# Optimization experiments

Measured on AMD Instinct MI355X. Metric: run time of the kernel, lower is better.

## Reference

```python
import jax, jax.numpy as jnp
import numpy as np

N_NODES = 50000
N_EDGES = 600000
DIM = 128
VOCAB = 512
PAD_ID = 0
LN_EPS = 1e-5


def setup_inputs() -> dict:
    key = jax.random.key(0)
    ks = jax.random.split(key, 8)
    node_ids = jax.random.randint(ks[0], (N_NODES,), 0, VOCAB, dtype=jnp.int32)
    edge_index = jax.random.randint(ks[1], (2, N_EDGES), 0, N_NODES, dtype=jnp.int32)
    edge_weight = jax.random.uniform(ks[2], (N_EDGES,), dtype=jnp.float32)
    # embedding with padding row zeroed (padding_idx semantics)
    emb = jax.random.normal(ks[3], (VOCAB, DIM), dtype=jnp.float32) * 0.05
    emb = emb.at[PAD_ID].set(0.0)
    s = 1.0 / np.sqrt(DIM)
    W1 = jax.random.normal(ks[4], (DIM, DIM), dtype=jnp.float32) * s
    b1 = jnp.zeros((DIM,), jnp.float32)
    W2 = jax.random.normal(ks[5], (DIM, DIM), dtype=jnp.float32) * s
    b2 = jnp.zeros((DIM,), jnp.float32)
    return {
        "node_ids": node_ids, "edge_index": edge_index, "edge_weight": edge_weight,
        "emb": emb, "W1": W1, "b1": b1, "W2": W2, "b2": b2,
        "gamma1": jnp.ones((DIM,), jnp.float32), "beta1": jnp.zeros((DIM,), jnp.float32),
        "gamma2": jnp.ones((DIM,), jnp.float32), "beta2": jnp.zeros((DIM,), jnp.float32),
    }


def _gcn_conv(x, row, col, ew, W, b, n_nodes):
    """PyG GCNConv: normalize=True, add_self_loops=True, improved=False.
    Aggregation j->i: edge (row=src j, col=dst i)."""
    h = x @ W  # [N, out]
    # add self loops with weight 1
    loop = jnp.arange(n_nodes, dtype=row.dtype)
    row_f = jnp.concatenate([row, loop])
    col_f = jnp.concatenate([col, loop])
    ew_f = jnp.concatenate([ew, jnp.ones((n_nodes,), ew.dtype)])
    # symmetric degree normalization (deg over destination index)
    deg = jax.ops.segment_sum(ew_f, col_f, num_segments=n_nodes)
    dis = jnp.where(deg > 0, jax.lax.rsqrt(jnp.maximum(deg, 1e-12)), 0.0)
    norm = dis[row_f] * ew_f * dis[col_f]  # [E+N]
    msg = norm[:, None] * h[row_f]  # gather + scale  [E+N, out]
    out = jax.ops.segment_sum(msg, col_f, num_segments=n_nodes)  # scatter-add
    return out + b


def _layer_norm(x, gamma, beta):
    mu = jnp.mean(x, axis=-1, keepdims=True)
    var = jnp.mean(jnp.square(x - mu), axis=-1, keepdims=True)
    return (x - mu) * jax.lax.rsqrt(var + LN_EPS) * gamma + beta


def reference(node_ids, edge_index, edge_weight, emb, W1, b1, W2, b2,
              gamma1, beta1, gamma2, beta2):
    row, col = edge_index[0], edge_index[1]
    x = emb[node_ids]  # [N, D]
    x1 = _gcn_conv(x, row, col, edge_weight, W1, b1, N_NODES)
    x = _layer_norm(x + x1, gamma1, beta1)  # dropout is identity in eval
    x2 = _gcn_conv(x, row, col, edge_weight, W2, b2, N_NODES)
    x = _layer_norm(x + x2, gamma2, beta2)
    return x
```

## Files before the change

### kernel.cpp

```cpp
#include <hip/hip_runtime.h>

#define N_NODES 50000
#define N_EDGES 600000
#define DIM     128
#define VOCAB   512
#define LN_EPS  1e-5f
#define FIXS    16777216.0f

typedef unsigned int uint;
typedef unsigned long long ull;
typedef unsigned short ushort;
typedef __attribute__((ext_vector_type(8))) short s8v;
typedef __attribute__((ext_vector_type(4))) float f4v;
typedef __attribute__((ext_vector_type(4))) int   i4v;
typedef __attribute__((ext_vector_type(4))) uint  u4v;
typedef __attribute__((ext_vector_type(2))) int   i2v;
typedef __attribute__((ext_vector_type(4))) float fv4;
typedef __attribute__((ext_vector_type(2))) float f2v;

__device__ __forceinline__ uint f2bf(float f) {
    uint u = __float_as_uint(f);
    return (u + 0x7fffu + ((u >> 16) & 1u)) >> 16;
}
__device__ __forceinline__ float bf_lo(uint p) { return __uint_as_float(p << 16); }
__device__ __forceinline__ float bf_hi(uint p) { return __uint_as_float(p & 0xffff0000u); }

__global__ void deg_rank_kernel(const int* __restrict__ ei, const float* __restrict__ ew,
                                ull* pack, ushort* __restrict__ rank, int E) {
    int e0 = (blockIdx.x * blockDim.x + threadIdx.x) * 8;
    if (e0 >= E) return;
    i4v c0 = __builtin_nontemporal_load((const i4v*)(ei + E + e0));
    i4v c1 = __builtin_nontemporal_load((const i4v*)(ei + E + e0 + 4));
    fv4 w0 = __builtin_nontemporal_load((const fv4*)(ew + e0));
    fv4 w1 = __builtin_nontemporal_load((const fv4*)(ew + e0 + 4));
    int   c[8] = {c0.x, c0.y, c0.z, c0.w, c1.x, c1.y, c1.z, c1.w};
    float w[8] = {w0.x, w0.y, w0.z, w0.w, w1.x, w1.y, w1.z, w1.w};
    ull r[8];
    #pragma unroll
    for (int k = 0; k < 8; k++) {
        ull a = (1ull << 32) | (ull)(uint)__float2int_rn(w[k] * FIXS);
        r[k] = atomicAdd(&pack[c[k]], a);
    }
    u4v o;
    o.x = (uint)(r[0] >> 32) | ((uint)(r[1] >> 32) << 16);
    o.y = (uint)(r[2] >> 32) | ((uint)(r[3] >> 32) << 16);
    o.z = (uint)(r[4] >> 32) | ((uint)(r[5] >> 32) << 16);
    o.w = (uint)(r[6] >> 32) | ((uint)(r[7] >> 32) << 16);
    __builtin_nontemporal_store(o, (u4v*)(rank + e0));
}

__global__ void scan_a(const ull* __restrict__ pack,
                       float* dis, int* row_ptr, int* bsum, int n) {
    __shared__ int sd[1024];
    int t = threadIdx.x;
    int i = blockIdx.x * 1024 + t;
    int v = 0;
    if (i < n) {
        ull pv = pack[i];
        v = (int)(pv >> 32);
        dis[i] = rsqrtf(1.0f + (float)(uint)(pv & 0xffffffffu) * (1.0f / FIXS));
    }
    sd[t] = v;
    __syncthreads();
    for (int off = 1; off < 1024; off <<= 1) {
        int add = (t >= off) ? sd[t - off] : 0;
        __syncthreads();
        sd[t] += add;
        __syncthreads();
    }
    if (i < n) row_ptr[i] = sd[t] - v;
    if (t == 1023) bsum[blockIdx.x] = sd[t];
}

__global__ void scan_c(int* row_ptr, const int* __restrict__ bsum,
                       int n, int E, int nb) {
    __shared__ int ofs_s;
    int t = threadIdx.x;
    if (t < 64) {
        int v = (t < nb && t < (int)blockIdx.x) ? bsum[t] : 0;
        #pragma unroll
        for (int o = 32; o > 0; o >>= 1) v += __shfl_xor(v, o, 64);
        if (t == 0) ofs_s = v;
    }
    __syncthreads();
    int i = blockIdx.x * 1024 + t;
    if (i < n) row_ptr[i] += ofs_s;
    if (i == 0) row_ptr[n] = E;
}

__global__ void scatter_kernel(const int* __restrict__ ei, const float* __restrict__ ew,
                               const float* __restrict__ dis, const int* __restrict__ nid,
                               const int* __restrict__ row_ptr, const ushort* __restrict__ rank,
                               int2* __restrict__ epack, int E) {
    int e = blockIdx.x * blockDim.x + threadIdx.x;
    if (e < E) {
        int s = ei[e];
        int c = ei[E + e];
        int pos = row_ptr[c] + (int)rank[e];
        uint ids = (uint)s | ((uint)nid[s] << 16);
        float wp = dis[s] * ew[e];
        i2v rec = {(int)ids, __float_as_int(wp)};
        __builtin_nontemporal_store(rec, (i2v*)(epack + pos));
    }
}

__global__ __launch_bounds__(256) void mm1_prepack(const float* __restrict__ X,
                                                   const float* __restrict__ W,
                                                   uint* __restrict__ Hb, int M,
                                                   const float* __restrict__ W2,
                                                   ushort* __restrict__ Wp) {
    __shared__ float Wt[32 * 128];
    __shared__ float Xt[64 * 36];
    int tid = threadIdx.x;
    int nmm = (M + 63) / 64;
    if ((int)blockIdx.x >= nmm) {
        int o = (blockIdx.x - nmm) * 256 + tid;
        int j = o & 7, lane = (o >> 3) & 63, chunk = o >> 9;
        int kc = chunk & 3, nc = chunk >> 2;
        int k = kc * 32 + (lane >> 4) * 8 + j;
        int n = nc * 16 + (lane & 15);
        Wp[o] = (ushort)f2bf(W2[k * 128 + n]);
        return;
    }
    int tx = tid & 31, ty = tid >> 5;
    int r0 = blockIdx.x * 64;
    float acc[8][4];
    #pragma unroll
    for (int j = 0; j < 8; j++)
        #pragma unroll
        for (int c = 0; c < 4; c++) acc[j][c] = 0.f;

    for (int kb = 0; kb < 128; kb += 32) {
        __syncthreads();
        #pragma unroll
        for (int q = 0; q < 4; q++) {
            int f = q * 256 + tid;
            ((float4*)Wt)[f] = *(const float4*)(W + kb * 128 + f * 4);
        }
        #pragma unroll
        for (int q = 0; q < 2; q++) {
            int f = q * 256 + tid;
            int row = f >> 3, cs = f & 7;
            int gr = r0 + row;
            float4 xv = make_float4(0.f, 0.f, 0.f, 0.f);
            if (gr < M) xv = *(const float4*)(X + (size_t)gr * 128 + kb + cs * 4);
            *(float4*)(Xt + row * 36 + cs * 4) = xv;
        }
        __syncthreads();
        #pragma unroll
        for (int k = 0; k < 32; k += 4) {
            float wv[4][4];
            #pragma unroll
            for (int kk = 0; kk < 4; kk++) {
                float4 t4 = *(const float4*)(Wt + (k + kk) * 128 + tx * 4);
                wv[kk][0] = t4.x; wv[kk][1] = t4.y; wv[kk][2] = t4.z; wv[kk][3] = t4.w;
            }
            #pragma unroll
            for (int j = 0; j < 8; j++) {
                float4 xv = *(const float4*)(Xt + (ty * 8 + j) * 36 + k);
                float xs[4] = {xv.x, xv.y, xv.z, xv.w};
                #pragma unroll
                for (int kk = 0; kk < 4; kk++)
                    #pragma unroll
                    for (int c = 0; c < 4; c++)
                        acc[j][c] = fmaf(xs[kk], wv[kk][c], acc[j][c]);
            }
        }
    }
    #pragma unroll
    for (int j = 0; j < 8; j++) {
        int gr = r0 + ty * 8 + j;
        if (gr < M) {
            uint p0 = f2bf(acc[j][0]) | (f2bf(acc[j][1]) << 16);
            uint p1 = f2bf(acc[j][2]) | (f2bf(acc[j][3]) << 16);
            ((uint2*)Hb)[(size_t)gr * 32 + tx] = make_uint2(p0, p1);
        }
    }
}

__global__ __launch_bounds__(256) void mm2_mfma(const uint* __restrict__ Xb,
                                                const ushort* __restrict__ Wp,
                                                ushort* __restrict__ H, int M) {
    int wid = (blockIdx.x * 256 + threadIdx.x) >> 6;
    int lane = threadIdx.x & 63;
    int r0 = wid * 16;
    if (r0 >= M) return;
    int quad = lane >> 4, lo = lane & 15;
    const uint* xrow = Xb + (size_t)(r0 + lo) * 64 + quad * 4;
    s8v a[4];
    #pragma unroll
    for (int kc = 0; kc < 4; kc++) a[kc] = *(const s8v*)(xrow + kc * 16);
    #pragma unroll
    for (int nc = 0; nc < 8; nc++) {
        f4v acc = {0.f, 0.f, 0.f, 0.f};
        #pragma unroll
        for (int kc = 0; kc < 4; kc++) {
            s8v b = *(const s8v*)(Wp + (size_t)((nc * 4 + kc) * 64 + lane) * 8);
            acc = __builtin_amdgcn_mfma_f32_16x16x32_bf16(a[kc], b, acc, 0, 0, 0);
        }
        ushort* hp = H + (size_t)(r0 + quad * 4) * 128 + nc * 16 + lo;
        #pragma unroll
        for (int r = 0; r < 4; r++)
            hp[(size_t)r * 128] = (ushort)f2bf(acc[r]);
    }
}

template<int SHIFT, bool RESID_BF, bool OUT_BF>
__global__ __launch_bounds__(256) void agg_ln(const int* __restrict__ row_ptr,
                                              const int2* __restrict__ epack,
                                              const float* __restrict__ dis,
                                              const uint* __restrict__ hb,
                                              const int* __restrict__ nid,
                                              const void* __restrict__ resid,
                                              const float* __restrict__ bias,
                                              const float* __restrict__ gamma,
                                              const float* __restrict__ beta,
                                              void* __restrict__ out, int n) {
    int i = (blockIdx.x * 256 + threadIdx.x) >> 6;
    int lane = threadIdx.x & 63;
    if (i >= n) return;
    int iw = __builtin_amdgcn_readfirstlane(i);
    int hri = nid ? nid[iw] : iw;
    float dl = dis[iw];
    uint ps = hb[(size_t)hri * 64 + lane];
    float sx[4] = {dl * bf_lo(ps), 0.f, 0.f, 0.f};
    float sy[4] = {dl * bf_hi(ps), 0.f, 0.f, 0.f};
    int e0 = row_ptr[iw], e1 = row_ptr[iw + 1];
    for (int j = e0; j < e1; j += 8) {
        i2v er[8];
        #pragma unroll
        for (int k = 0; k < 8; k++) {
            int idx = (j + k < e1) ? j + k : e0;
            er[k] = __builtin_nontemporal_load((const i2v*)(epack + idx));
        }
        uint qv[8];
        #pragma unroll
        for (int k = 0; k < 8; k++)
            qv[k] = hb[(size_t)(((uint)er[k].x >> SHIFT) & 0xffffu) * 64 + lane];
        #pragma unroll
        for (int k = 0; k < 8; k++) {
            float w = (j + k < e1) ? __int_as_float(er[k].y) : 0.f;
            sx[k & 3] += w * bf_lo(qv[k]);
            sy[k & 3] += w * bf_hi(qv[k]);
        }
    }
    float acc0 = (sx[0] + sx[1]) + (sx[2] + sx[3]);
    float acc1 = (sy[0] + sy[1]) + (sy[2] + sy[3]);
    float2 xr;
    if (RESID_BF) {
        uint pr = __builtin_nontemporal_load((const uint*)resid + (size_t)hri * 64 + lane);
        xr = make_float2(bf_lo(pr), bf_hi(pr));
    } else {
        xr = ((const float2*)resid)[(size_t)hri * 64 + lane];
    }
    float2 bi = ((const float2*)bias)[lane];
    float v0 = xr.x + dl * acc0 + bi.x;
    float v1 = xr.y + dl * acc1 + bi.y;
    float s1 = v0 + v1, s2 = v0 * v0 + v1 * v1;
    #pragma unroll
    for (int o = 32; o > 0; o >>= 1) {
        s1 += __shfl_xor(s1, o, 64);
        s2 += __shfl_xor(s2, o, 64);
    }
    float mu   = s1 * (1.0f / DIM);
    float var  = s2 * (1.0f / DIM) - mu * mu;
    float rstd = rsqrtf(var + LN_EPS);
    float2 ga = ((const float2*)gamma)[lane];
    float2 be = ((const float2*)beta)[lane];
    float o0 = (v0 - mu) * rstd * ga.x + be.x;
    float o1 = (v1 - mu) * rstd * ga.y + be.y;
    if (OUT_BF) {
        __builtin_nontemporal_store(f2bf(o0) | (f2bf(o1) << 16),
                                    (uint*)out + (size_t)i * 64 + lane);
    } else {
        f2v ov = {o0, o1};
        __builtin_nontemporal_store(ov, (f2v*)((float2*)out + (size_t)i * 64 + lane));
    }
}

extern "C" void kernel_launch(void* const* d_in, const int* in_sizes, int n_in,
                              void* d_out, int out_size, void* d_ws, size_t ws_size,
                              hipStream_t stream) {
    const int*   node_ids = (const int*)  d_in[0];
    const int*   ei       = (const int*)  d_in[1];
    const float* ew       = (const float*)d_in[2];
    const float* emb      = (const float*)d_in[3];
    const float* W1       = (const float*)d_in[4];
    const float* b1       = (const float*)d_in[5];
    const float* W2       = (const float*)d_in[6];
    const float* b2       = (const float*)d_in[7];
    const float* g1       = (const float*)d_in[8];
    const float* be1      = (const float*)d_in[9];
    const float* g2       = (const float*)d_in[10];
    const float* be2      = (const float*)d_in[11];
    float* out = (float*)d_out;

    char* p = (char*)d_ws;
    auto alloc = [&](size_t bytes) {
        char* r = p;
        p += (bytes + 255) & ~(size_t)255;
        return r;
    };
    uint*   h2b     = (uint*)  alloc((size_t)N_NODES * 64 * 4);
    uint*   x1b     = (uint*)  alloc((size_t)N_NODES * 64 * 4);
    uint*   hembB   = (uint*)  alloc((size_t)VOCAB * 64 * 4);
    ushort* Wp      = (ushort*)alloc((size_t)128 * 128 * 2);
    ull*    pack    = (ull*)   alloc((size_t)N_NODES * 8);
    float*  disv    = (float*) alloc((size_t)N_NODES * 4);
    int*    row_ptr = (int*)   alloc((size_t)(N_NODES + 1) * 4);
    ushort* rank    = (ushort*)alloc((size_t)N_EDGES * 2);
    int*    bsum    = (int*)   alloc(64 * 4);
    int2*   epack   = (int2*)  alloc((size_t)N_EDGES * 8);

    int nb = (N_NODES + 1023) / 1024;

    (void)hipMemsetAsync(pack, 0, (size_t)N_NODES * 8, stream);
    deg_rank_kernel<<<(N_EDGES / 8 + 255) / 256, 256, 0, stream>>>(ei, ew, pack, rank, N_EDGES);
    scan_a<<<nb, 1024, 0, stream>>>(pack, disv, row_ptr, bsum, N_NODES);
    scan_c<<<nb, 1024, 0, stream>>>(row_ptr, bsum, N_NODES, N_EDGES, nb);
    scatter_kernel<<<(N_EDGES + 255) / 256, 256, 0, stream>>>(ei, ew, disv, node_ids,
                                                              row_ptr, rank, epack, N_EDGES);

    mm1_prepack<<<(VOCAB + 63) / 64 + 64, 256, 0, stream>>>(emb, W1, hembB, VOCAB, W2, Wp);
    agg_ln<16, false, true><<<(N_NODES + 3) / 4, 256, 0, stream>>>(
        row_ptr, epack, disv, hembB, node_ids, emb, b1, g1, be1, x1b, N_NODES);

    mm2_mfma<<<(N_NODES / 16 + 3) / 4, 256, 0, stream>>>(x1b, Wp, (ushort*)h2b, N_NODES);
    agg_ln<0, true, false><<<(N_NODES + 3) / 4, 256, 0, stream>>>(
        row_ptr, epack, disv, h2b, nullptr, x1b, b2, g2, be2, out, N_NODES);
}
```

Before: 226.4 us.

## Store layer-2 features as FP8 and fuse degree count with mm1 prepack

The mm2 output H is now written as FP8 (one byte per element) rather than bf16. The second aggregation gathers 2 bytes per lane per neighbour instead of 4, which halves the random-gather traffic of the dominant kernel. Separately, the degree/rank atomic kernel is merged into the same launch as the embedding matmul and W2 prepack, removing one kernel launch. FP8 storage of the pre-aggregation features lowers accuracy, which risks exceeding the tolerance.

```diff
diff --git a/kernel.cpp b/kernel.cpp
--- a/kernel.cpp
+++ b/kernel.cpp
@@ -10,6 +10,7 @@
 typedef unsigned int uint;
 typedef unsigned long long ull;
 typedef unsigned short ushort;
+typedef unsigned char uchar;
 typedef __attribute__((ext_vector_type(8))) short s8v;
 typedef __attribute__((ext_vector_type(4))) float f4v;
 typedef __attribute__((ext_vector_type(4))) int   i4v;
@@ -25,96 +26,49 @@
 __device__ __forceinline__ float bf_lo(uint p) { return __uint_as_float(p << 16); }
 __device__ __forceinline__ float bf_hi(uint p) { return __uint_as_float(p & 0xffff0000u); }
 
-__global__ void deg_rank_kernel(const int* __restrict__ ei, const float* __restrict__ ew,
-                                ull* pack, ushort* __restrict__ rank, int E) {
-    int e0 = (blockIdx.x * blockDim.x + threadIdx.x) * 8;
-    if (e0 >= E) return;
-    i4v c0 = __builtin_nontemporal_load((const i4v*)(ei + E + e0));
-    i4v c1 = __builtin_nontemporal_load((const i4v*)(ei + E + e0 + 4));
-    fv4 w0 = __builtin_nontemporal_load((const fv4*)(ew + e0));
-    fv4 w1 = __builtin_nontemporal_load((const fv4*)(ew + e0 + 4));
-    int   c[8] = {c0.x, c0.y, c0.z, c0.w, c1.x, c1.y, c1.z, c1.w};
-    float w[8] = {w0.x, w0.y, w0.z, w0.w, w1.x, w1.y, w1.z, w1.w};
-    ull r[8];
-    #pragma unroll
-    for (int k = 0; k < 8; k++) {
-        ull a = (1ull << 32) | (ull)(uint)__float2int_rn(w[k] * FIXS);
-        r[k] = atomicAdd(&pack[c[k]], a);
-    }
-    u4v o;
-    o.x = (uint)(r[0] >> 32) | ((uint)(r[1] >> 32) << 16);
-    o.y = (uint)(r[2] >> 32) | ((uint)(r[3] >> 32) << 16);
-    o.z = (uint)(r[4] >> 32) | ((uint)(r[5] >> 32) << 16);
-    o.w = (uint)(r[6] >> 32) | ((uint)(r[7] >> 32) << 16);
-    __builtin_nontemporal_store(o, (u4v*)(rank + e0));
-}
-
-__global__ void scan_a(const ull* __restrict__ pack,
-                       float* dis, int* row_ptr, int* bsum, int n) {
-    __shared__ int sd[1024];
-    int t = threadIdx.x;
-    int i = blockIdx.x * 1024 + t;
-    int v = 0;
-    if (i < n) {
-        ull pv = pack[i];
-        v = (int)(pv >> 32);
-        dis[i] = rsqrtf(1.0f + (float)(uint)(pv & 0xffffffffu) * (1.0f / FIXS));
-    }
-    sd[t] = v;
-    __syncthreads();
-    for (int off = 1; off < 1024; off <<= 1) {
-        int add = (t >= off) ? sd[t - off] : 0;
-        __syncthreads();
-        sd[t] += add;
-        __syncthreads();
-    }
-    if (i < n) row_ptr[i] = sd[t] - v;
-    if (t == 1023) bsum[blockIdx.x] = sd[t];
-}
-
-__global__ void scan_c(int* row_ptr, const int* __restrict__ bsum,
-                       int n, int E, int nb) {
-    __shared__ int ofs_s;
-    int t = threadIdx.x;
-    if (t < 64) {
-        int v = (t < nb && t < (int)blockIdx.x) ? bsum[t] : 0;
-        #pragma unroll
-        for (int o = 32; o > 0; o >>= 1) v += __shfl_xor(v, o, 64);
-        if (t == 0) ofs_s = v;
-    }
-    __syncthreads();
-    int i = blockIdx.x * 1024 + t;
-    if (i < n) row_ptr[i] += ofs_s;
-    if (i == 0) row_ptr[n] = E;
-}
-
-__global__ void scatter_kernel(const int* __restrict__ ei, const float* __restrict__ ew,
-                               const float* __restrict__ dis, const int* __restrict__ nid,
-                               const int* __restrict__ row_ptr, const ushort* __restrict__ rank,
-                               int2* __restrict__ epack, int E) {
-    int e = blockIdx.x * blockDim.x + threadIdx.x;
-    if (e < E) {
-        int s = ei[e];
-        int c = ei[E + e];
-        int pos = row_ptr[c] + (int)rank[e];
-        uint ids = (uint)s | ((uint)nid[s] << 16);
-        float wp = dis[s] * ew[e];
-        i2v rec = {(int)ids, __float_as_int(wp)};
-        __builtin_nontemporal_store(rec, (i2v*)(epack + pos));
-    }
-}
-
-__global__ __launch_bounds__(256) void mm1_prepack(const float* __restrict__ X,
-                                                   const float* __restrict__ W,
-                                                   uint* __restrict__ Hb, int M,
-                                                   const float* __restrict__ W2,
-                                                   ushort* __restrict__ Wp) {
+__device__ __forceinline__ uchar f2fp8(float v) {
+    return (uchar)(__builtin_amdgcn_cvt_pk_fp8_f32(v, v, 0, false) & 0xff);
+}
+__device__ __forceinline__ f2v fp8x2_to_f2(uint packed2) {
+    return __builtin_amdgcn_cvt_pk_f32_fp8((int)packed2, false);
+}
+
+__global__ __launch_bounds__(256) void deg_mm1_kernel(
+        const int* __restrict__ ei, const float* __restrict__ ew,
+        ull* pack, ushort* __restrict__ rank, int E,
+        const float* __restrict__ X, const float* __restrict__ W,
+        uint* __restrict__ Hb, int M,
+        const float* __restrict__ W2, ushort* __restrict__ Wp) {
     __shared__ float Wt[32 * 128];
     __shared__ float Xt[64 * 36];
     int tid = threadIdx.x;
+    int nbDeg = (E / 8 + 255) / 256;
     int nmm = (M + 63) / 64;
-    if ((int)blockIdx.x >= nmm) {
-        int o = (blockIdx.x - nmm) * 256 + tid;
+    if ((int)blockIdx.x < nbDeg) {
+        int e0 = (blockIdx.x * 256 + tid) * 8;
+        if (e0 >= E) return;
+        i4v c0 = __builtin_nontemporal_load((const i4v*)(ei + E + e0));
+        i4v c1 = __builtin_nontemporal_load((const i4v*)(ei + E + e0 + 4));
+        fv4 w0 = __builtin_nontemporal_load((const fv4*)(ew + e0));
+        fv4 w1 = __builtin_nontemporal_load((const fv4*)(ew + e0 + 4));
+        int   c[8] = {c0.x, c0.y, c0.z, c0.w, c1.x, c1.y, c1.z, c1.w};
+        float w[8] = {w0.x, w0.y, w0.z, w0.w, w1.x, w1.y, w1.z, w1.w};
+        ull r[8];
+        #pragma unroll
+        for (int k = 0; k < 8; k++) {
+            ull a = (1ull << 32) | (ull)(uint)__float2int_rn(w[k] * FIXS);
+            r[k] = atomicAdd(&pack[c[k]], a);
+        }
+        u4v o;
+        o.x = (uint)(r[0] >> 32) | ((uint)(r[1] >> 32) << 16);
+        o.y = (uint)(r[2] >> 32) | ((uint)(r[3] >> 32) << 16);
+        o.z = (uint)(r[4] >> 32) | ((uint)(r[5] >> 32) << 16);
+        o.w = (uint)(r[6] >> 32) | ((uint)(r[7] >> 32) << 16);
+        __builtin_nontemporal_store(o, (u4v*)(rank + e0));
+        return;
+    }
+    if ((int)blockIdx.x >= nbDeg + nmm) {
+        int o = (blockIdx.x - nbDeg - nmm) * 256 + tid;
         int j = o & 7, lane = (o >> 3) & 63, chunk = o >> 9;
         int kc = chunk & 3, nc = chunk >> 2;
         int k = kc * 32 + (lane >> 4) * 8 + j;
@@ -122,8 +76,9 @@
         Wp[o] = (ushort)f2bf(W2[k * 128 + n]);
         return;
     }
+    int bx = blockIdx.x - nbDeg;
     int tx = tid & 31, ty = tid >> 5;
-    int r0 = blockIdx.x * 64;
+    int r0 = bx * 64;
     float acc[8][4];
     #pragma unroll
     for (int j = 0; j < 8; j++)
@@ -178,9 +133,64 @@
     }
 }
 
+__global__ void scan_a(const ull* __restrict__ pack,
+                       float* dis, int* row_ptr, int* bsum, int n) {
+    __shared__ int sd[1024];
+    int t = threadIdx.x;
+    int i = blockIdx.x * 1024 + t;
+    int v = 0;
+    if (i < n) {
+        ull pv = pack[i];
+        v = (int)(pv >> 32);
+        dis[i] = rsqrtf(1.0f + (float)(uint)(pv & 0xffffffffu) * (1.0f / FIXS));
+    }
+    sd[t] = v;
+    __syncthreads();
+    for (int off = 1; off < 1024; off <<= 1) {
+        int add = (t >= off) ? sd[t - off] : 0;
+        __syncthreads();
+        sd[t] += add;
+        __syncthreads();
+    }
+    if (i < n) row_ptr[i] = sd[t] - v;
+    if (t == 1023) bsum[blockIdx.x] = sd[t];
+}
+
+__global__ void scan_c(int* row_ptr, const int* __restrict__ bsum,
+                       int n, int E, int nb) {
+    __shared__ int ofs_s;
+    int t = threadIdx.x;
+    if (t < 64) {
+        int v = (t < nb && t < (int)blockIdx.x) ? bsum[t] : 0;
+        #pragma unroll
+        for (int o = 32; o > 0; o >>= 1) v += __shfl_xor(v, o, 64);
+        if (t == 0) ofs_s = v;
+    }
+    __syncthreads();
+    int i = blockIdx.x * 1024 + t;
+    if (i < n) row_ptr[i] += ofs_s;
+    if (i == 0) row_ptr[n] = E;
+}
+
+__global__ void scatter_kernel(const int* __restrict__ ei, const float* __restrict__ ew,
+                               const float* __restrict__ dis, const int* __restrict__ nid,
+                               const int* __restrict__ row_ptr, const ushort* __restrict__ rank,
+                               int2* __restrict__ epack, int E) {
+    int e = blockIdx.x * blockDim.x + threadIdx.x;
+    if (e < E) {
+        int s = ei[e];
+        int c = ei[E + e];
+        int pos = row_ptr[c] + (int)rank[e];
+        uint ids = (uint)s | ((uint)nid[s] << 16);
+        float wp = dis[s] * ew[e];
+        i2v rec = {(int)ids, __float_as_int(wp)};
+        __builtin_nontemporal_store(rec, (i2v*)(epack + pos));
+    }
+}
+
 __global__ __launch_bounds__(256) void mm2_mfma(const uint* __restrict__ Xb,
                                                 const ushort* __restrict__ Wp,
-                                                ushort* __restrict__ H, int M) {
+                                                uchar* __restrict__ H8, int M) {
     int wid = (blockIdx.x * 256 + threadIdx.x) >> 6;
     int lane = threadIdx.x & 63;
     int r0 = wid * 16;
@@ -198,18 +208,18 @@
             s8v b = *(const s8v*)(Wp + (size_t)((nc * 4 + kc) * 64 + lane) * 8);
             acc = __builtin_amdgcn_mfma_f32_16x16x32_bf16(a[kc], b, acc, 0, 0, 0);
         }
-        ushort* hp = H + (size_t)(r0 + quad * 4) * 128 + nc * 16 + lo;
+        uchar* hp = H8 + (size_t)(r0 + quad * 4) * 128 + nc * 16 + lo;
         #pragma unroll
         for (int r = 0; r < 4; r++)
-            hp[(size_t)r * 128] = (ushort)f2bf(acc[r]);
-    }
-}
-
-template<int SHIFT, bool RESID_BF, bool OUT_BF>
+            hp[(size_t)r * 128] = f2fp8(acc[r]);
+    }
+}
+
+template<int SHIFT, bool RESID_BF, bool OUT_BF, bool GF8>
 __global__ __launch_bounds__(256) void agg_ln(const int* __restrict__ row_ptr,
                                               const int2* __restrict__ epack,
                                               const float* __restrict__ dis,
-                                              const uint* __restrict__ hb,
+                                              const void* __restrict__ hb,
                                               const int* __restrict__ nid,
                                               const void* __restrict__ resid,
                                               const float* __restrict__ bias,
@@ -222,9 +232,17 @@
     int iw = __builtin_amdgcn_readfirstlane(i);
     int hri = nid ? nid[iw] : iw;
     float dl = dis[iw];
-    uint ps = hb[(size_t)hri * 64 + lane];
-    float sx[4] = {dl * bf_lo(ps), 0.f, 0.f, 0.f};
-    float sy[4] = {dl * bf_hi(ps), 0.f, 0.f, 0.f};
+    float slo, shi;
+    if (GF8) {
+        uint ps = ((const ushort*)hb)[(size_t)hri * 64 + lane];
+        f2v d = fp8x2_to_f2(ps);
+        slo = d.x; shi = d.y;
+    } else {
+        uint ps = ((const uint*)hb)[(size_t)hri * 64 + lane];
+        slo = bf_lo(ps); shi = bf_hi(ps);
+    }
+    float sx[4] = {dl * slo, 0.f, 0.f, 0.f};
+    float sy[4] = {dl * shi, 0.f, 0.f, 0.f};
     int e0 = row_ptr[iw], e1 = row_ptr[iw + 1];
     for (int j = e0; j < e1; j += 8) {
         i2v er[8];
@@ -235,13 +253,19 @@
         }
         uint qv[8];
         #pragma unroll
-        for (int k = 0; k < 8; k++)
-            qv[k] = hb[(size_t)(((uint)er[k].x >> SHIFT) & 0xffffu) * 64 + lane];
+        for (int k = 0; k < 8; k++) {
+            size_t row = ((uint)er[k].x >> SHIFT) & 0xffffu;
+            qv[k] = GF8 ? (uint)((const ushort*)hb)[row * 64 + lane]
+                        : ((const uint*)hb)[row * 64 + lane];
+        }
         #pragma unroll
         for (int k = 0; k < 8; k++) {
             float w = (j + k < e1) ? __int_as_float(er[k].y) : 0.f;
-            sx[k & 3] += w * bf_lo(qv[k]);
-            sy[k & 3] += w * bf_hi(qv[k]);
+            float lo, hi;
+            if (GF8) { f2v d = fp8x2_to_f2(qv[k]); lo = d.x; hi = d.y; }
+            else     { lo = bf_lo(qv[k]); hi = bf_hi(qv[k]); }
+            sx[k & 3] += w * lo;
+            sy[k & 3] += w * hi;
         }
     }
     float acc0 = (sx[0] + sx[1]) + (sx[2] + sx[3]);
@@ -301,7 +325,7 @@
         p += (bytes + 255) & ~(size_t)255;
         return r;
     };
-    uint*   h2b     = (uint*)  alloc((size_t)N_NODES * 64 * 4);
+    uchar*  h8      = (uchar*) alloc((size_t)N_NODES * DIM);
     uint*   x1b     = (uint*)  alloc((size_t)N_NODES * 64 * 4);
     uint*   hembB   = (uint*)  alloc((size_t)VOCAB * 64 * 4);
     ushort* Wp      = (ushort*)alloc((size_t)128 * 128 * 2);
@@ -313,19 +337,21 @@
     int2*   epack   = (int2*)  alloc((size_t)N_EDGES * 8);
 
     int nb = (N_NODES + 1023) / 1024;
+    int nbDeg = (N_EDGES / 8 + 255) / 256;
+    int nmm = (VOCAB + 63) / 64;
 
     (void)hipMemsetAsync(pack, 0, (size_t)N_NODES * 8, stream);
-    deg_rank_kernel<<<(N_EDGES / 8 + 255) / 256, 256, 0, stream>>>(ei, ew, pack, rank, N_EDGES);
+    deg_mm1_kernel<<<nbDeg + nmm + 64, 256, 0, stream>>>(
+        ei, ew, pack, rank, N_EDGES, emb, W1, hembB, VOCAB, W2, Wp);
     scan_a<<<nb, 1024, 0, stream>>>(pack, disv, row_ptr, bsum, N_NODES);
     scan_c<<<nb, 1024, 0, stream>>>(row_ptr, bsum, N_NODES, N_EDGES, nb);
     scatter_kernel<<<(N_EDGES + 255) / 256, 256, 0, stream>>>(ei, ew, disv, node_ids,
                                                               row_ptr, rank, epack, N_EDGES);
 
-    mm1_prepack<<<(VOCAB + 63) / 64 + 64, 256, 0, stream>>>(emb, W1, hembB, VOCAB, W2, Wp);
-    agg_ln<16, false, true><<<(N_NODES + 3) / 4, 256, 0, stream>>>(
+    agg_ln<16, false, true, false><<<(N_NODES + 3) / 4, 256, 0, stream>>>(
         row_ptr, epack, disv, hembB, node_ids, emb, b1, g1, be1, x1b, N_NODES);
 
-    mm2_mfma<<<(N_NODES / 16 + 3) / 4, 256, 0, stream>>>(x1b, Wp, (ushort*)h2b, N_NODES);
-    agg_ln<0, true, false><<<(N_NODES + 3) / 4, 256, 0, stream>>>(
-        row_ptr, epack, disv, h2b, nullptr, x1b, b2, g2, be2, out, N_NODES);
-}
+    mm2_mfma<<<(N_NODES / 16 + 3) / 4, 256, 0, stream>>>(x1b, Wp, h8, N_NODES);
+    agg_ln<0, true, false, true><<<(N_NODES + 3) / 4, 256, 0, stream>>>(
+        row_ptr, epack, disv, h8, nullptr, x1b, b2, g2, be2, out, N_NODES);
+}
```

After: 216.8 us. 1.04x faster.
